# Kernel tuning notes

Hardware: AMD Instinct MI355X
Metric: run time of the kernel (lower is better)

The kernel has to match this reference:

```python
import jax, jax.numpy as jnp
import numpy as np

DX = 0.1  # grid spacing (init arg dx); dy == dx
NX = 4096
NY = 4096


def _pad_bc(X, left, right, top, bottom):
    # X: [1, 1, Nx, Ny]; pad last axis with left/right values, then second-to-last with top/bottom.
    B, C, Nx, Ny = X.shape
    l = jnp.broadcast_to(left, (B, C, Nx, 1)).astype(X.dtype)
    r = jnp.broadcast_to(right, (B, C, Nx, 1)).astype(X.dtype)
    X = jnp.concatenate([l, X, r], axis=3)
    t = jnp.broadcast_to(top, (B, C, 1, Ny + 2)).astype(X.dtype)
    bo = jnp.broadcast_to(bottom, (B, C, 1, Ny + 2)).astype(X.dtype)
    return jnp.concatenate([t, X, bo], axis=2)


def _laplacian(Xp):
    # 5-point stencil, equivalent to conv2d with [[0,1,0],[1,-4,1],[0,1,0]]/dx^2 (valid padding).
    inv_dx2 = 1.0 / (DX * DX)
    return (
        Xp[:, :, :-2, 1:-1]
        + Xp[:, :, 2:, 1:-1]
        + Xp[:, :, 1:-1, :-2]
        + Xp[:, :, 1:-1, 2:]
        - 4.0 * Xp[:, :, 1:-1, 1:-1]
    ) * inv_dx2


def setup_inputs() -> dict:
    key = jax.random.key(0)
    k1, k2 = jax.random.split(key)
    state = jax.random.normal(k1, (1, 2, NX, NY), dtype=jnp.float32)
    bc = jax.random.uniform(k2, (1, 2, 4), dtype=jnp.float32)
    a_org = jnp.asarray(-2.0, dtype=jnp.float32)
    b_org = jnp.asarray(-2.0, dtype=jnp.float32)
    k_org = jnp.asarray(-2.0, dtype=jnp.float32)
    return {"state": state, "bc": bc, "a_org": a_org, "b_org": b_org, "k_org": k_org}


def reference(state, bc, a_org, b_org, k_org):
    a = jax.nn.sigmoid(a_org) * 0.01
    b = jax.nn.sigmoid(b_org) * 0.01
    k = jax.nn.sigmoid(k_org) * 0.01

    U = state[:, :1]  # [1,1,Nx,Ny]
    V = state[:, 1:]

    U_ = _pad_bc(U, bc[0, 0, 0], bc[0, 0, 1], bc[0, 0, 2], bc[0, 0, 3])
    V_ = _pad_bc(V, bc[0, 1, 0], bc[0, 1, 1], bc[0, 1, 2], bc[0, 1, 3])

    delta_u = _laplacian(U_)
    delta_v = _laplacian(V_)

    dUdt = a * delta_u + U - U ** 3 - V - k
    dVdt = b * delta_v + U - V
    return jnp.concatenate([dUdt, dVdt], axis=1)
```

## Files before the change

kernel.cpp:

```cpp
#include <hip/hip_runtime.h>

#define NXD 4096
#define NYD 4096
#define ROWS 8

typedef float f32x4 __attribute__((ext_vector_type(4)));

__global__ __launch_bounds__(256) void DiffReactParamPDE_85478439125433_kernel(
    const float* __restrict__ state,
    const float* __restrict__ bc,
    const float* __restrict__ a_org,
    const float* __restrict__ b_org,
    const float* __restrict__ k_org,
    float* __restrict__ out)
{
    const float inv_dx2 = 100.0f;

    const float a = 0.01f / (1.0f + expf(-a_org[0]));
    const float b = 0.01f / (1.0f + expf(-b_org[0]));
    const float k = 0.01f / (1.0f + expf(-k_org[0]));

    const float uL = bc[0], uR = bc[1], uT = bc[2], uB = bc[3];
    const float vL = bc[4], vR = bc[5], vT = bc[6], vB = bc[7];

    const int lane = threadIdx.x & 63;
    const int j0 = (blockIdx.x * 256 + threadIdx.x) * 4;
    const int i0 = blockIdx.y * ROWS;

    const float* __restrict__ U = state;
    const float* __restrict__ V = state + (size_t)NXD * NYD;
    float* __restrict__ dU = out;
    float* __restrict__ dV = out + (size_t)NXD * NYD;

    const float4 fuT = make_float4(uT, uT, uT, uT), fuB = make_float4(uB, uB, uB, uB);
    const float4 fvT = make_float4(vT, vT, vT, vT), fvB = make_float4(vB, vB, vB, vB);

#define LD4(P, ROW) (*(const float4*)((P) + (size_t)(ROW) * NYD + j0))

    float4 um, uc, up, vm, vc, vp;
    if (i0 > 0) { um = LD4(U, i0 - 1); vm = LD4(V, i0 - 1); }
    else        { um = fuT;            vm = fvT; }
    uc = LD4(U, i0); vc = LD4(V, i0);
    if (i0 + 1 < NXD) { up = LD4(U, i0 + 1); vp = LD4(V, i0 + 1); }
    else              { up = fuB;            vp = fvB; }

    float eLu = uL, eRu = uR, eLv = vL, eRv = vR;
    if (lane == 0 && j0 > 0) {
        eLu = U[(size_t)i0 * NYD + j0 - 1];
        eLv = V[(size_t)i0 * NYD + j0 - 1];
    }
    if (lane == 63 && j0 + 4 < NYD) {
        eRu = U[(size_t)i0 * NYD + j0 + 4];
        eRv = V[(size_t)i0 * NYD + j0 + 4];
    }

#pragma unroll
    for (int r = 0; r < ROWS; ++r) {
        const int row = i0 + r;

        float4 un = fuB, vn = fvB;
        float eLu_n = uL, eRu_n = uR, eLv_n = vL, eRv_n = vR;
        if (r < ROWS - 1) {
            const int rn = row + 2;
            if (rn < NXD) { un = LD4(U, rn); vn = LD4(V, rn); }
            if (lane == 0 && j0 > 0) {
                eLu_n = U[(size_t)(row + 1) * NYD + j0 - 1];
                eLv_n = V[(size_t)(row + 1) * NYD + j0 - 1];
            }
            if (lane == 63 && j0 + 4 < NYD) {
                eRu_n = U[(size_t)(row + 1) * NYD + j0 + 4];
                eRv_n = V[(size_t)(row + 1) * NYD + j0 + 4];
            }
        }

        float ulft = __shfl_up(uc.w, 1);   if (lane == 0)  ulft = eLu;
        float urgt = __shfl_down(uc.x, 1); if (lane == 63) urgt = eRu;
        float vlft = __shfl_up(vc.w, 1);   if (lane == 0)  vlft = eLv;
        float vrgt = __shfl_down(vc.x, 1); if (lane == 63) vrgt = eRv;

        const float lu0 = (um.x + up.x + ulft + uc.y - 4.0f * uc.x) * inv_dx2;
        const float lu1 = (um.y + up.y + uc.x + uc.z - 4.0f * uc.y) * inv_dx2;
        const float lu2 = (um.z + up.z + uc.y + uc.w - 4.0f * uc.z) * inv_dx2;
        const float lu3 = (um.w + up.w + uc.z + urgt - 4.0f * uc.w) * inv_dx2;

        const float lv0 = (vm.x + vp.x + vlft + vc.y - 4.0f * vc.x) * inv_dx2;
        const float lv1 = (vm.y + vp.y + vc.x + vc.z - 4.0f * vc.y) * inv_dx2;
        const float lv2 = (vm.z + vp.z + vc.y + vc.w - 4.0f * vc.z) * inv_dx2;
        const float lv3 = (vm.w + vp.w + vc.z + vrgt - 4.0f * vc.w) * inv_dx2;

        f32x4 duo, dvo;
        duo.x = a * lu0 + uc.x - uc.x * uc.x * uc.x - vc.x - k;
        duo.y = a * lu1 + uc.y - uc.y * uc.y * uc.y - vc.y - k;
        duo.z = a * lu2 + uc.z - uc.z * uc.z * uc.z - vc.z - k;
        duo.w = a * lu3 + uc.w - uc.w * uc.w * uc.w - vc.w - k;

        dvo.x = b * lv0 + uc.x - vc.x;
        dvo.y = b * lv1 + uc.y - vc.y;
        dvo.z = b * lv2 + uc.z - vc.z;
        dvo.w = b * lv3 + uc.w - vc.w;

        const size_t bo = (size_t)row * NYD + j0;
        __builtin_nontemporal_store(duo, (f32x4*)(dU + bo));
        __builtin_nontemporal_store(dvo, (f32x4*)(dV + bo));

        um = uc; uc = up; up = un;
        vm = vc; vc = vp; vp = vn;
        eLu = eLu_n; eRu = eRu_n; eLv = eLv_n; eRv = eRv_n;
    }
#undef LD4
}

extern "C" void kernel_launch(void* const* d_in, const int* in_sizes, int n_in,
                              void* d_out, int out_size, void* d_ws, size_t ws_size,
                              hipStream_t stream) {
    const float* state = (const float*)d_in[0];
    const float* bc    = (const float*)d_in[1];
    const float* a_org = (const float*)d_in[2];
    const float* b_org = (const float*)d_in[3];
    const float* k_org = (const float*)d_in[4];
    float* out = (float*)d_out;

    dim3 block(256, 1, 1);
    dim3 grid(NYD / (4 * 256), NXD / ROWS, 1);
    DiffReactParamPDE_85478439125433_kernel<<<grid, block, 0, stream>>>(
        state, bc, a_org, b_org, k_org, out);
}
```

Before: 246.0 us.

## Replace rolling row window with triple-buffered independent row loads for more memory parallelism

Each output row now loads its own three stencil rows into one of three rotating register sets, issued three rows ahead, so many independent loads are in flight at once. Halo values for all rows and the scalar parameters are fetched up front after the first loads are issued. The per-row reuse of neighbouring rows in registers is dropped, so each thread issues about three times as many row loads, relying on cache hits, and register pressure grows.

```diff
diff --git a/kernel.cpp b/kernel.cpp
--- a/kernel.cpp
+++ b/kernel.cpp
@@ -16,13 +16,6 @@
 {
     const float inv_dx2 = 100.0f;
 
-    const float a = 0.01f / (1.0f + expf(-a_org[0]));
-    const float b = 0.01f / (1.0f + expf(-b_org[0]));
-    const float k = 0.01f / (1.0f + expf(-k_org[0]));
-
-    const float uL = bc[0], uR = bc[1], uT = bc[2], uB = bc[3];
-    const float vL = bc[4], vR = bc[5], vT = bc[6], vB = bc[7];
-
     const int lane = threadIdx.x & 63;
     const int j0 = (blockIdx.x * 256 + threadIdx.x) * 4;
     const int i0 = blockIdx.y * ROWS;
@@ -32,81 +25,94 @@
     float* __restrict__ dU = out;
     float* __restrict__ dV = out + (size_t)NXD * NYD;
 
-    const float4 fuT = make_float4(uT, uT, uT, uT), fuB = make_float4(uB, uB, uB, uB);
-    const float4 fvT = make_float4(vT, vT, vT, vT), fvB = make_float4(vB, vB, vB, vB);
-
 #define LD4(P, ROW) (*(const float4*)((P) + (size_t)(ROW) * NYD + j0))
 
-    float4 um, uc, up, vm, vc, vp;
-    if (i0 > 0) { um = LD4(U, i0 - 1); vm = LD4(V, i0 - 1); }
-    else        { um = fuT;            vm = fvT; }
-    uc = LD4(U, i0); vc = LD4(V, i0);
-    if (i0 + 1 < NXD) { up = LD4(U, i0 + 1); vp = LD4(V, i0 + 1); }
-    else              { up = fuB;            vp = fvB; }
+#define LDROW(row, um, uc, up, vm, vc, vp) do {                         \
+        const int rm_ = ((row) == 0) ? 0 : (row) - 1;                   \
+        const int rp_ = ((row) + 1 == NXD) ? (row) : (row) + 1;         \
+        um = LD4(U, rm_); uc = LD4(U, (row)); up = LD4(U, rp_);         \
+        vm = LD4(V, rm_); vc = LD4(V, (row)); vp = LD4(V, rp_);         \
+    } while (0)
 
-    float eLu = uL, eRu = uR, eLv = vL, eRv = vR;
+    float4 umA, ucA, upA, vmA, vcA, vpA;
+    float4 umB, ucB, upB, vmB, vcB, vpB;
+    float4 umC, ucC, upC, vmC, vcC, vpC;
+
+    LDROW(i0 + 0, umA, ucA, upA, vmA, vcA, vpA);
+    LDROW(i0 + 1, umB, ucB, upB, vmB, vcB, vpB);
+    LDROW(i0 + 2, umC, ucC, upC, vmC, vcC, vpC);
+
+    const float uL = bc[0], uR = bc[1], uT = bc[2], uB = bc[3];
+    const float vL = bc[4], vR = bc[5], vT = bc[6], vB = bc[7];
+    const float a = 0.01f / (1.0f + expf(-a_org[0]));
+    const float b = 0.01f / (1.0f + expf(-b_org[0]));
+    const float k = 0.01f / (1.0f + expf(-k_org[0]));
+    const float4 fuT = make_float4(uT, uT, uT, uT), fuB4 = make_float4(uB, uB, uB, uB);
+    const float4 fvT = make_float4(vT, vT, vT, vT), fvB4 = make_float4(vB, vB, vB, vB);
+
+    float eU[ROWS], eV[ROWS];
+#pragma unroll
+    for (int r = 0; r < ROWS; ++r) {
+        eU[r] = (lane == 0) ? uL : uR;
+        eV[r] = (lane == 0) ? vL : vR;
+    }
     if (lane == 0 && j0 > 0) {
-        eLu = U[(size_t)i0 * NYD + j0 - 1];
-        eLv = V[(size_t)i0 * NYD + j0 - 1];
+#pragma unroll
+        for (int r = 0; r < ROWS; ++r) {
+            eU[r] = U[(size_t)(i0 + r) * NYD + j0 - 1];
+            eV[r] = V[(size_t)(i0 + r) * NYD + j0 - 1];
+        }
     }
     if (lane == 63 && j0 + 4 < NYD) {
-        eRu = U[(size_t)i0 * NYD + j0 + 4];
-        eRv = V[(size_t)i0 * NYD + j0 + 4];
+#pragma unroll
+        for (int r = 0; r < ROWS; ++r) {
+            eU[r] = U[(size_t)(i0 + r) * NYD + j0 + 4];
+            eV[r] = V[(size_t)(i0 + r) * NYD + j0 + 4];
+        }
     }
 
-#pragma unroll
-    for (int r = 0; r < ROWS; ++r) {
-        const int row = i0 + r;
+#define DOROW(r, um, uc, up, vm, vc, vp) do {                                    \
+        const int row_ = i0 + (r);                                               \
+        float4 umz = um, vmz = vm, upz = up, vpz = vp;                           \
+        if (row_ == 0)       { umz = fuT;  vmz = fvT;  }                         \
+        if (row_ + 1 == NXD) { upz = fuB4; vpz = fvB4; }                         \
+        float ulft = __shfl_up(uc.w, 1);   if (lane == 0)  ulft = eU[r];         \
+        float urgt = __shfl_down(uc.x, 1); if (lane == 63) urgt = eU[r];         \
+        float vlft = __shfl_up(vc.w, 1);   if (lane == 0)  vlft = eV[r];         \
+        float vrgt = __shfl_down(vc.x, 1); if (lane == 63) vrgt = eV[r];         \
+        const float lu0 = (umz.x + upz.x + ulft + uc.y - 4.0f * uc.x) * inv_dx2; \
+        const float lu1 = (umz.y + upz.y + uc.x + uc.z - 4.0f * uc.y) * inv_dx2; \
+        const float lu2 = (umz.z + upz.z + uc.y + uc.w - 4.0f * uc.z) * inv_dx2; \
+        const float lu3 = (umz.w + upz.w + uc.z + urgt - 4.0f * uc.w) * inv_dx2; \
+        const float lv0 = (vmz.x + vpz.x + vlft + vc.y - 4.0f * vc.x) * inv_dx2; \
+        const float lv1 = (vmz.y + vpz.y + vc.x + vc.z - 4.0f * vc.y) * inv_dx2; \
+        const float lv2 = (vmz.z + vpz.z + vc.y + vc.w - 4.0f * vc.z) * inv_dx2; \
+        const float lv3 = (vmz.w + vpz.w + vc.z + vrgt - 4.0f * vc.w) * inv_dx2; \
+        f32x4 duo, dvo;                                                          \
+        duo.x = a * lu0 + uc.x - uc.x * uc.x * uc.x - vc.x - k;                  \
+        duo.y = a * lu1 + uc.y - uc.y * uc.y * uc.y - vc.y - k;                  \
+        duo.z = a * lu2 + uc.z - uc.z * uc.z * uc.z - vc.z - k;                  \
+        duo.w = a * lu3 + uc.w - uc.w * uc.w * uc.w - vc.w - k;                  \
+        dvo.x = b * lv0 + uc.x - vc.x;                                           \
+        dvo.y = b * lv1 + uc.y - vc.y;                                           \
+        dvo.z = b * lv2 + uc.z - vc.z;                                           \
+        dvo.w = b * lv3 + uc.w - vc.w;                                           \
+        const size_t bo_ = (size_t)row_ * NYD + j0;                              \
+        __builtin_nontemporal_store(duo, (f32x4*)(dU + bo_));                    \
+        __builtin_nontemporal_store(dvo, (f32x4*)(dV + bo_));                    \
+    } while (0)
 
-        float4 un = fuB, vn = fvB;
-        float eLu_n = uL, eRu_n = uR, eLv_n = vL, eRv_n = vR;
-        if (r < ROWS - 1) {
-            const int rn = row + 2;
-            if (rn < NXD) { un = LD4(U, rn); vn = LD4(V, rn); }
-            if (lane == 0 && j0 > 0) {
-                eLu_n = U[(size_t)(row + 1) * NYD + j0 - 1];
-                eLv_n = V[(size_t)(row + 1) * NYD + j0 - 1];
-            }
-            if (lane == 63 && j0 + 4 < NYD) {
-                eRu_n = U[(size_t)(row + 1) * NYD + j0 + 4];
-                eRv_n = V[(size_t)(row + 1) * NYD + j0 + 4];
-            }
-        }
+    DOROW(0, umA, ucA, upA, vmA, vcA, vpA);  LDROW(i0 + 3, umA, ucA, upA, vmA, vcA, vpA);
+    DOROW(1, umB, ucB, upB, vmB, vcB, vpB);  LDROW(i0 + 4, umB, ucB, upB, vmB, vcB, vpB);
+    DOROW(2, umC, ucC, upC, vmC, vcC, vpC);  LDROW(i0 + 5, umC, ucC, upC, vmC, vcC, vpC);
+    DOROW(3, umA, ucA, upA, vmA, vcA, vpA);  LDROW(i0 + 6, umA, ucA, upA, vmA, vcA, vpA);
+    DOROW(4, umB, ucB, upB, vmB, vcB, vpB);  LDROW(i0 + 7, umB, ucB, upB, vmB, vcB, vpB);
+    DOROW(5, umC, ucC, upC, vmC, vcC, vpC);
+    DOROW(6, umA, ucA, upA, vmA, vcA, vpA);
+    DOROW(7, umB, ucB, upB, vmB, vcB, vpB);
 
-        float ulft = __shfl_up(uc.w, 1);   if (lane == 0)  ulft = eLu;
-        float urgt = __shfl_down(uc.x, 1); if (lane == 63) urgt = eRu;
-        float vlft = __shfl_up(vc.w, 1);   if (lane == 0)  vlft = eLv;
-        float vrgt = __shfl_down(vc.x, 1); if (lane == 63) vrgt = eRv;
-
-        const float lu0 = (um.x + up.x + ulft + uc.y - 4.0f * uc.x) * inv_dx2;
-        const float lu1 = (um.y + up.y + uc.x + uc.z - 4.0f * uc.y) * inv_dx2;
-        const float lu2 = (um.z + up.z + uc.y + uc.w - 4.0f * uc.z) * inv_dx2;
-        const float lu3 = (um.w + up.w + uc.z + urgt - 4.0f * uc.w) * inv_dx2;
-
-        const float lv0 = (vm.x + vp.x + vlft + vc.y - 4.0f * vc.x) * inv_dx2;
-        const float lv1 = (vm.y + vp.y + vc.x + vc.z - 4.0f * vc.y) * inv_dx2;
-        const float lv2 = (vm.z + vp.z + vc.y + vc.w - 4.0f * vc.z) * inv_dx2;
-        const float lv3 = (vm.w + vp.w + vc.z + vrgt - 4.0f * vc.w) * inv_dx2;
-
-        f32x4 duo, dvo;
-        duo.x = a * lu0 + uc.x - uc.x * uc.x * uc.x - vc.x - k;
-        duo.y = a * lu1 + uc.y - uc.y * uc.y * uc.y - vc.y - k;
-        duo.z = a * lu2 + uc.z - uc.z * uc.z * uc.z - vc.z - k;
-        duo.w = a * lu3 + uc.w - uc.w * uc.w * uc.w - vc.w - k;
-
-        dvo.x = b * lv0 + uc.x - vc.x;
-        dvo.y = b * lv1 + uc.y - vc.y;
-        dvo.z = b * lv2 + uc.z - vc.z;
-        dvo.w = b * lv3 + uc.w - vc.w;
-
-        const size_t bo = (size_t)row * NYD + j0;
-        __builtin_nontemporal_store(duo, (f32x4*)(dU + bo));
-        __builtin_nontemporal_store(dvo, (f32x4*)(dV + bo));
-
-        um = uc; uc = up; up = un;
-        vm = vc; vc = vp; vp = vn;
-        eLu = eLu_n; eRu = eRu_n; eLv = eLv_n; eRv = eRv_n;
-    }
+#undef DOROW
+#undef LDROW
 #undef LD4
 }
 
```

Result: no change. 243.3 us (-1.1%).

## Stage stencil rows in LDS via async global_load_lds instead of register rolling

Applied to the files above, without the earlier changes.

Each block now async-copies its band of TR+2 rows of U and V straight into shared memory with global_load_lds, then computes the 5-point stencil from LDS. Horizontal neighbours are read from LDS instead of wave shuffles, and the tile edges come from per-row scalar halo loads. The grid is flattened to 1D, and the stores switch from nontemporal to plain. The aim is to issue all loads up front for more memory-level parallelism. In exchange it uses about 80KB of LDS per block, which limits occupancy, and re-reads the halo rows.

```diff
diff --git a/kernel.cpp b/kernel.cpp
--- a/kernel.cpp
+++ b/kernel.cpp
@@ -2,9 +2,13 @@
 
 #define NXD 4096
 #define NYD 4096
-#define ROWS 8
+#define TR 8
+#define TC 1024
 
 typedef float f32x4 __attribute__((ext_vector_type(4)));
+
+#define AS_GLB const __attribute__((address_space(1))) unsigned int
+#define AS_LDS __attribute__((address_space(3))) unsigned int
 
 __global__ __launch_bounds__(256) void DiffReactParamPDE_85478439125433_kernel(
     const float* __restrict__ state,
@@ -16,67 +20,86 @@
 {
     const float inv_dx2 = 100.0f;
 
-    const float a = 0.01f / (1.0f + expf(-a_org[0]));
-    const float b = 0.01f / (1.0f + expf(-b_org[0]));
-    const float k = 0.01f / (1.0f + expf(-k_org[0]));
+    __shared__ float sU[TR + 2][TC];
+    __shared__ float sV[TR + 2][TC];
 
-    const float uL = bc[0], uR = bc[1], uT = bc[2], uB = bc[3];
-    const float vL = bc[4], vR = bc[5], vT = bc[6], vB = bc[7];
-
-    const int lane = threadIdx.x & 63;
-    const int j0 = (blockIdx.x * 256 + threadIdx.x) * 4;
-    const int i0 = blockIdx.y * ROWS;
+    const int tid   = threadIdx.x;
+    const int tileX = blockIdx.x & 3;
+    const int band  = blockIdx.x >> 2;
+    const int j0    = tileX * TC + tid * 4;
+    const int i0    = band * TR;
 
     const float* __restrict__ U = state;
     const float* __restrict__ V = state + (size_t)NXD * NYD;
     float* __restrict__ dU = out;
     float* __restrict__ dV = out + (size_t)NXD * NYD;
 
-    const float4 fuT = make_float4(uT, uT, uT, uT), fuB = make_float4(uB, uB, uB, uB);
-    const float4 fvT = make_float4(vT, vT, vT, vT), fvB = make_float4(vB, vB, vB, vB);
-
-#define LD4(P, ROW) (*(const float4*)((P) + (size_t)(ROW) * NYD + j0))
-
-    float4 um, uc, up, vm, vc, vp;
-    if (i0 > 0) { um = LD4(U, i0 - 1); vm = LD4(V, i0 - 1); }
-    else        { um = fuT;            vm = fvT; }
-    uc = LD4(U, i0); vc = LD4(V, i0);
-    if (i0 + 1 < NXD) { up = LD4(U, i0 + 1); vp = LD4(V, i0 + 1); }
-    else              { up = fuB;            vp = fvB; }
-
-    float eLu = uL, eRu = uR, eLv = vL, eRv = vR;
-    if (lane == 0 && j0 > 0) {
-        eLu = U[(size_t)i0 * NYD + j0 - 1];
-        eLv = V[(size_t)i0 * NYD + j0 - 1];
-    }
-    if (lane == 63 && j0 + 4 < NYD) {
-        eRu = U[(size_t)i0 * NYD + j0 + 4];
-        eRv = V[(size_t)i0 * NYD + j0 + 4];
+#pragma unroll
+    for (int s = 0; s < TR + 2; ++s) {
+        int gr = i0 - 1 + s;
+        gr = (gr < 0) ? 0 : ((gr >= NXD) ? NXD - 1 : gr);
+        __builtin_amdgcn_global_load_lds(
+            (AS_GLB*)(U + (size_t)gr * NYD + j0),
+            (AS_LDS*)&sU[s][tid * 4], 16, 0, 0);
+        __builtin_amdgcn_global_load_lds(
+            (AS_GLB*)(V + (size_t)gr * NYD + j0),
+            (AS_LDS*)&sV[s][tid * 4], 16, 0, 0);
     }
 
+    const float uL = bc[0], uR = bc[1], uT = bc[2], uB = bc[3];
+    const float vL = bc[4], vR = bc[5], vT = bc[6], vB = bc[7];
+    const float a = 0.01f / (1.0f + expf(-a_org[0]));
+    const float b = 0.01f / (1.0f + expf(-b_org[0]));
+    const float k = 0.01f / (1.0f + expf(-k_org[0]));
+
+    float eu[TR], ev[TR];
 #pragma unroll
-    for (int r = 0; r < ROWS; ++r) {
+    for (int r = 0; r < TR; ++r) {
+        eu[r] = (tid == 0) ? uL : uR;
+        ev[r] = (tid == 0) ? vL : vR;
+    }
+    if (tid == 0 && tileX > 0) {
+        const int jl = tileX * TC - 1;
+#pragma unroll
+        for (int r = 0; r < TR; ++r) {
+            eu[r] = U[(size_t)(i0 + r) * NYD + jl];
+            ev[r] = V[(size_t)(i0 + r) * NYD + jl];
+        }
+    }
+    if (tid == 255 && tileX < 3) {
+        const int jr = tileX * TC + TC;
+#pragma unroll
+        for (int r = 0; r < TR; ++r) {
+            eu[r] = U[(size_t)(i0 + r) * NYD + jr];
+            ev[r] = V[(size_t)(i0 + r) * NYD + jr];
+        }
+    }
+
+    __syncthreads();
+
+    const float4 fuT = make_float4(uT, uT, uT, uT), fuB4 = make_float4(uB, uB, uB, uB);
+    const float4 fvT = make_float4(vT, vT, vT, vT), fvB4 = make_float4(vB, vB, vB, vB);
+
+#pragma unroll
+    for (int r = 0; r < TR; ++r) {
+        const int s   = r + 1;
         const int row = i0 + r;
+        const int c   = tid * 4;
 
-        float4 un = fuB, vn = fvB;
-        float eLu_n = uL, eRu_n = uR, eLv_n = vL, eRv_n = vR;
-        if (r < ROWS - 1) {
-            const int rn = row + 2;
-            if (rn < NXD) { un = LD4(U, rn); vn = LD4(V, rn); }
-            if (lane == 0 && j0 > 0) {
-                eLu_n = U[(size_t)(row + 1) * NYD + j0 - 1];
-                eLv_n = V[(size_t)(row + 1) * NYD + j0 - 1];
-            }
-            if (lane == 63 && j0 + 4 < NYD) {
-                eRu_n = U[(size_t)(row + 1) * NYD + j0 + 4];
-                eRv_n = V[(size_t)(row + 1) * NYD + j0 + 4];
-            }
-        }
+        float4 uc = *(const float4*)&sU[s][c];
+        float4 um = *(const float4*)&sU[s - 1][c];
+        float4 up = *(const float4*)&sU[s + 1][c];
+        float4 vc = *(const float4*)&sV[s][c];
+        float4 vm = *(const float4*)&sV[s - 1][c];
+        float4 vp = *(const float4*)&sV[s + 1][c];
 
-        float ulft = __shfl_up(uc.w, 1);   if (lane == 0)  ulft = eLu;
-        float urgt = __shfl_down(uc.x, 1); if (lane == 63) urgt = eRu;
-        float vlft = __shfl_up(vc.w, 1);   if (lane == 0)  vlft = eLv;
-        float vrgt = __shfl_down(vc.x, 1); if (lane == 63) vrgt = eRv;
+        if (row == 0)       { um = fuT;  vm = fvT;  }
+        if (row == NXD - 1) { up = fuB4; vp = fvB4; }
+
+        const float ulft = (tid == 0)   ? eu[r] : sU[s][c - 1];
+        const float urgt = (tid == 255) ? eu[r] : sU[s][c + 4];
+        const float vlft = (tid == 0)   ? ev[r] : sV[s][c - 1];
+        const float vrgt = (tid == 255) ? ev[r] : sV[s][c + 4];
 
         const float lu0 = (um.x + up.x + ulft + uc.y - 4.0f * uc.x) * inv_dx2;
         const float lu1 = (um.y + up.y + uc.x + uc.z - 4.0f * uc.y) * inv_dx2;
@@ -100,14 +123,9 @@
         dvo.w = b * lv3 + uc.w - vc.w;
 
         const size_t bo = (size_t)row * NYD + j0;
-        __builtin_nontemporal_store(duo, (f32x4*)(dU + bo));
-        __builtin_nontemporal_store(dvo, (f32x4*)(dV + bo));
-
-        um = uc; uc = up; up = un;
-        vm = vc; vc = vp; vp = vn;
-        eLu = eLu_n; eRu = eRu_n; eLv = eLv_n; eRv = eRv_n;
+        *(f32x4*)(dU + bo) = duo;
+        *(f32x4*)(dV + bo) = dvo;
     }
-#undef LD4
 }
 
 extern "C" void kernel_launch(void* const* d_in, const int* in_sizes, int n_in,
@@ -121,7 +139,7 @@
     float* out = (float*)d_out;
 
     dim3 block(256, 1, 1);
-    dim3 grid(NYD / (4 * 256), NXD / ROWS, 1);
+    dim3 grid((NYD / TC) * (NXD / TR), 1, 1);
     DiffReactParamPDE_85478439125433_kernel<<<grid, block, 0, stream>>>(
         state, bc, a_org, b_org, k_org, out);
 }
```

After: 245.7 us. About the same (-0.1%).
